# Performance work log

Hardware: AMD Instinct MI355X
Metric: run time of the kernel (lower is better)

## Reference

```python
import jax, jax.numpy as jnp
import numpy as np

B, T, D, H = 8, 1024, 512, 8
HD = D // H
EPS = 1e-5


def setup_inputs() -> dict:
    key = jax.random.key(0)
    ks = jax.random.split(key, 16)
    s = 0.02
    return {
        "query": jax.random.normal(ks[0], (B, T, D), jnp.float32),
        "key": jax.random.normal(ks[1], (B, T, D), jnp.float32),
        "value": jax.random.normal(ks[2], (B, T, D), jnp.float32),
        "frac": jax.random.uniform(ks[3], (B, T), jnp.float32),
        "Wq": jax.random.normal(ks[4], (D, D), jnp.float32) * s,
        "bq": jnp.zeros((D,), jnp.float32),
        "Wk": jax.random.normal(ks[5], (D, D), jnp.float32) * s,
        "bk": jnp.zeros((D,), jnp.float32),
        "Wv": jax.random.normal(ks[6], (D, D), jnp.float32) * s,
        "bv": jnp.zeros((D,), jnp.float32),
        "Wo": jax.random.normal(ks[7], (D, D), jnp.float32) * s,
        "bo": jnp.zeros((D,), jnp.float32),
        # alpha params are zeros in torch init; use small randn so the bias path is non-degenerate
        "alpha_pos": jax.random.normal(ks[8], (H,), jnp.float32) * 0.1,
        "alpha_neg": jax.random.normal(ks[9], (H,), jnp.float32) * 0.1,
        "gamma": jnp.asarray(1.0, jnp.float32),
        "delta": jnp.asarray(0.2, jnp.float32),
        "add_frac_bias": 1,
    }


def _zscore_last(t):
    # torch.std uses unbiased estimator (ddof=1)
    m = t.mean(axis=-1, keepdims=True)
    s = jnp.std(t, axis=-1, keepdims=True, ddof=1)
    return (t - m) / (s + EPS)


def reference(query, key, value, frac, Wq, bq, Wk, bk, Wv, bv, Wo, bo,
              alpha_pos, alpha_neg, gamma, delta, add_frac_bias):
    b, t, d = query.shape
    h = alpha_pos.shape[0]
    hd = d // h
    scale = hd ** -0.5

    def proj(x, W, bias):
        return (x @ W + bias).reshape(b, t, h, hd).transpose(0, 2, 1, 3)  # [B,H,T,hd]

    Q = proj(query, Wq, bq)
    K = proj(key, Wk, bk)
    V = proj(value, Wv, bv)

    logits = jnp.einsum('bhqd,bhkd->bhqk', Q, K) * scale  # [B,H,T,T]

    fi = frac[:, :, None]          # [B,T,1]
    fj = frac[:, None, :]          # [B,1,T]
    Dm = (fj - fi) * (fi * fj)     # [B,T,T]
    D_pos = jax.nn.relu(Dm)
    D_neg = -jax.nn.relu(-Dm)
    stoich = (alpha_pos[None, :, None, None] * D_pos[:, None]
              + alpha_neg[None, :, None, None] * D_neg[:, None])  # [B,H,T,T]

    logits_z = _zscore_last(logits)
    if add_frac_bias:
        attn = gamma * logits_z + delta * _zscore_last(stoich)
    else:
        attn = gamma * logits_z

    probs = jax.nn.softmax(attn, axis=-1)
    out = jnp.einsum('bhqk,bhkd->bhqd', probs, V)  # [B,H,T,hd]
    out = out.transpose(0, 2, 1, 3).reshape(b, t, d)
    return out @ Wo + bo
```

## Files before the change

kernel.cpp:

```cpp
#include <hip/hip_runtime.h>
#include <hip/hip_bf16.h>

#define EPS 1e-5f
#define FLASH_SMEM 72704

typedef short bf16x8 __attribute__((ext_vector_type(8)));
typedef float f32x4 __attribute__((ext_vector_type(4)));

#define GL16(gp, lp) __builtin_amdgcn_global_load_lds( \
    (const __attribute__((address_space(1))) void*)(gp), \
    (__attribute__((address_space(3))) void*)(lp), 16, 0, 0)

__device__ __forceinline__ unsigned short f2bf(float f) {
  union { float f; unsigned u; } v; v.f = f;
  return (unsigned short)((v.u + 0x7FFFu + ((v.u >> 16) & 1u)) >> 16);
}
__device__ __forceinline__ float bf2f(unsigned short u) {
  return __uint_as_float(((unsigned)u) << 16);
}

__global__ void wtrans4_kernel(const float* __restrict__ W0, const float* __restrict__ W1,
                               const float* __restrict__ W2, const float* __restrict__ W3,
                               unsigned short* __restrict__ T0, unsigned short* __restrict__ T1,
                               unsigned short* __restrict__ T2, unsigned short* __restrict__ T3) {
  __shared__ float tile[32][33];
  int z = blockIdx.z;
  const float* W = z == 0 ? W0 : z == 1 ? W1 : z == 2 ? W2 : W3;
  unsigned short* Wt = z == 0 ? T0 : z == 1 ? T1 : z == 2 ? T2 : T3;
  float scale = (z == 0) ? 0.125f : 1.0f;
  int n0 = blockIdx.x * 32, k0 = blockIdx.y * 32;
  int c = threadIdx.x & 31, r0 = threadIdx.x >> 5;
  #pragma unroll
  for (int rr = 0; rr < 32; rr += 8)
    tile[r0 + rr][c] = W[(k0 + r0 + rr) * 512 + n0 + c];
  __syncthreads();
  #pragma unroll
  for (int rr = 0; rr < 32; rr += 8)
    Wt[(n0 + r0 + rr) * 512 + k0 + c] = f2bf(tile[c][r0 + rr] * scale);
}

__global__ void frac_stats_kernel(const float* __restrict__ frac,
                                  float* __restrict__ fstats) {
  int wid = (int)((blockIdx.x * blockDim.x + threadIdx.x) >> 6);
  int ln = threadIdx.x & 63;
  if (wid >= 8192) return;
  int b = wid >> 10, q = wid & 1023;
  const float* fr = frac + b * 1024;
  float fq = fr[q];
  float sp = 0.f, sn = 0.f, sp2 = 0.f, sn2 = 0.f;
  for (int i = ln; i < 1024; i += 64) {
    float f = fr[i];
    float dm = (f - fq) * (fq * f);
    float p = fmaxf(dm, 0.f), nn = fminf(dm, 0.f);
    sp += p; sn += nn; sp2 += p * p; sn2 += nn * nn;
  }
  #pragma unroll
  for (int m = 32; m; m >>= 1) {
    sp += __shfl_xor(sp, m); sn += __shfl_xor(sn, m);
    sp2 += __shfl_xor(sp2, m); sn2 += __shfl_xor(sn2, m);
  }
  if (ln == 0) {
    float4 o; o.x = sp; o.y = sn; o.z = sp2; o.w = sn2;
    *(float4*)(fstats + (size_t)wid * 4) = o;
  }
}

__global__ __launch_bounds__(256) void qkv_gemm_kernel(
    const float* __restrict__ Aq, const float* __restrict__ Ak, const float* __restrict__ Av,
    const unsigned short* __restrict__ WqT, const unsigned short* __restrict__ WkT,
    const unsigned short* __restrict__ WvT,
    const float* __restrict__ bq, const float* __restrict__ bk, const float* __restrict__ bv,
    unsigned short* __restrict__ Qh, unsigned short* __restrict__ Kh,
    unsigned short* __restrict__ Ktr, unsigned short* __restrict__ Vt) {
  __shared__ unsigned short Al[2][128 * 32];
  __shared__ unsigned short Bl[2][128 * 32];
  const int L = blockIdx.x;
  const int xcd = L & 7, sl = L >> 3;
  const int xb = sl & 3;
  const int P = (sl >> 2) * 8 + xcd;
  const int yb = P & 63, z = P >> 6;

  const float* A = z == 0 ? Aq : z == 1 ? Ak : Av;
  const unsigned short* Bt = z == 0 ? WqT : z == 1 ? WkT : WvT;
  const float* bias = z == 0 ? bq : z == 1 ? bk : bv;
  const float bscale = (z == 0) ? 0.125f : 1.0f;

  const int tid = threadIdx.x, ln = tid & 63, wv = tid >> 6;
  const int m0 = yb * 128, n0 = xb * 128;
  const int wr = wv >> 1, wc = wv & 1;
  const int arow = tid >> 1;
  const int agh = (tid & 1) * 2;

  auto stageB = [&](int kt, int buf) {
    int kb = kt * 32;
    #pragma unroll
    for (int u = 0; u < 2; ++u) {
      int n = tid + u * 256;
      int Lrow = n >> 2, kcs = n & 3;
      int kc = kcs ^ (Lrow & 3);
      GL16(Bt + (size_t)(n0 + Lrow) * 512 + kb + kc * 8, &Bl[buf][n * 8]);
    }
  };
  auto loadA = [&](int kt, float4* la) {
    const float* src = A + (size_t)(m0 + arow) * 512 + kt * 32 + agh * 8;
    la[0] = *(const float4*)(src);
    la[1] = *(const float4*)(src + 4);
    la[2] = *(const float4*)(src + 8);
    la[3] = *(const float4*)(src + 12);
  };
  auto writeA = [&](int buf, const float4* la) {
    #pragma unroll
    for (int G = 0; G < 2; ++G) {
      union { bf16x8 v; unsigned short u[8]; } pk;
      float4 a = la[2 * G], b2 = la[2 * G + 1];
      pk.u[0] = f2bf(a.x); pk.u[1] = f2bf(a.y); pk.u[2] = f2bf(a.z); pk.u[3] = f2bf(a.w);
      pk.u[4] = f2bf(b2.x); pk.u[5] = f2bf(b2.y); pk.u[6] = f2bf(b2.z); pk.u[7] = f2bf(b2.w);
      int dg = (agh + G) ^ (arow & 3);
      *(bf16x8*)(&Al[buf][arow * 32 + dg * 8]) = pk.v;
    }
  };

  f32x4 acc[4][4] = {};
  float4 la[4];
  loadA(0, la); writeA(0, la);
  stageB(0, 0);
  for (int kt = 0; kt < 16; ++kt) {
    __syncthreads();
    if (kt < 15) { loadA(kt + 1, la); stageB(kt + 1, (kt + 1) & 1); }
    const unsigned short* a_ = Al[kt & 1];
    const unsigned short* b_ = Bl[kt & 1];
    const int kc = ln >> 4;
    bf16x8 afr[4], bfr[4];
    #pragma unroll
    for (int m = 0; m < 4; ++m) {
      int r = wr * 64 + m * 16 + (ln & 15);
      afr[m] = *(const bf16x8*)(a_ + r * 32 + ((kc ^ (r & 3)) * 8));
    }
    #pragma unroll
    for (int n = 0; n < 4; ++n) {
      int r = wc * 64 + n * 16 + (ln & 15);
      bfr[n] = *(const bf16x8*)(b_ + r * 32 + ((kc ^ (r & 3)) * 8));
    }
    #pragma unroll
    for (int m = 0; m < 4; ++m)
      #pragma unroll
      for (int n = 0; n < 4; ++n)
        acc[m][n] = __builtin_amdgcn_mfma_f32_16x16x32_bf16(afr[m], bfr[n], acc[m][n], 0, 0, 0);
    if (kt < 15) writeA((kt + 1) & 1, la);
  }

  #pragma unroll
  for (int m = 0; m < 4; ++m) {
    #pragma unroll
    for (int n = 0; n < 4; ++n) {
      int gm0 = m0 + wr * 64 + m * 16 + (ln >> 4) * 4;
      int gn = n0 + wc * 64 + n * 16 + (ln & 15);
      float bvv = bias[gn] * bscale;
      int hh = gn >> 6, d = gn & 63;
      if (z < 2) {
        unsigned short* o = z == 0 ? Qh : Kh;
        #pragma unroll
        for (int i = 0; i < 4; ++i) {
          int gm = gm0 + i;
          int bb = gm >> 10, t = gm & 1023;
          o[(size_t)((bb * 8 + hh) * 1024 + t) * 64 + d] = f2bf(acc[m][n][i] + bvv);
        }
        if (z == 1) {
          int bb = gm0 >> 10, t = gm0 & 1023;
          ushort4 pk;
          pk.x = f2bf(acc[m][n][0] + bvv);
          pk.y = f2bf(acc[m][n][1] + bvv);
          pk.z = f2bf(acc[m][n][2] + bvv);
          pk.w = f2bf(acc[m][n][3] + bvv);
          *(ushort4*)(Ktr + (size_t)((bb * 8 + hh) * 64 + d) * 1024 + t) = pk;
        }
      } else {
        int bb = gm0 >> 10, t = gm0 & 1023;
        int k5 = t & 31;
        int pos = (t & ~31) + ((k5 >> 2) & 3) * 8 + ((k5 >> 4) & 1) * 4;
        ushort4 pk;
        pk.x = f2bf(acc[m][n][0] + bvv);
        pk.y = f2bf(acc[m][n][1] + bvv);
        pk.z = f2bf(acc[m][n][2] + bvv);
        pk.w = f2bf(acc[m][n][3] + bvv);
        *(ushort4*)(Vt + (size_t)((bb * 8 + hh) * 64 + d) * 1024 + pos) = pk;
      }
    }
  }
}

__global__ __launch_bounds__(256) void gemm_out_kernel(
    const unsigned short* __restrict__ A,
    const unsigned short* __restrict__ Bt,
    const float* __restrict__ bias,
    float* __restrict__ out) {
  __shared__ unsigned short Al[2][128 * 32];
  __shared__ unsigned short Bl[2][128 * 32];
  const int L = blockIdx.x;
  const int xcd = L & 7, sl = L >> 3;
  const int xb = sl & 3, yb = (sl >> 2) * 8 + xcd;
  const int tid = threadIdx.x, ln = tid & 63, wv = tid >> 6;
  const int m0 = yb * 128, n0 = xb * 128;
  const int wr = wv >> 1, wc = wv & 1;

  auto stage = [&](int kt, int buf) {
    int kb = kt * 32;
    #pragma unroll
    for (int u = 0; u < 2; ++u) {
      int n = tid + u * 256;
      int Lrow = n >> 2, kcs = n & 3;
      int kc = kcs ^ (Lrow & 3);
      GL16(A + (size_t)(m0 + Lrow) * 512 + kb + kc * 8, &Al[buf][n * 8]);
      GL16(Bt + (size_t)(n0 + Lrow) * 512 + kb + kc * 8, &Bl[buf][n * 8]);
    }
  };

  f32x4 acc[4][4] = {};
  stage(0, 0);
  for (int kt = 0; kt < 16; ++kt) {
    __syncthreads();
    if (kt < 15) stage(kt + 1, (kt + 1) & 1);
    const unsigned short* a_ = Al[kt & 1];
    const unsigned short* b_ = Bl[kt & 1];
    const int kc = ln >> 4;
    bf16x8 afr[4], bfr[4];
    #pragma unroll
    for (int m = 0; m < 4; ++m) {
      int r = wr * 64 + m * 16 + (ln & 15);
      afr[m] = *(const bf16x8*)(a_ + r * 32 + ((kc ^ (r & 3)) * 8));
    }
    #pragma unroll
    for (int n = 0; n < 4; ++n) {
      int r = wc * 64 + n * 16 + (ln & 15);
      bfr[n] = *(const bf16x8*)(b_ + r * 32 + ((kc ^ (r & 3)) * 8));
    }
    #pragma unroll
    for (int m = 0; m < 4; ++m)
      #pragma unroll
      for (int n = 0; n < 4; ++n)
        acc[m][n] = __builtin_amdgcn_mfma_f32_16x16x32_bf16(afr[m], bfr[n], acc[m][n], 0, 0, 0);
  }
  #pragma unroll
  for (int m = 0; m < 4; ++m)
    #pragma unroll
    for (int n = 0; n < 4; ++n) {
      int gm0 = m0 + wr * 64 + m * 16 + (ln >> 4) * 4;
      int gn = n0 + wc * 64 + n * 16 + (ln & 15);
      float bvv = bias[gn];
      #pragma unroll
      for (int i = 0; i < 4; ++i)
        out[(size_t)(gm0 + i) * 512 + gn] = acc[m][n][i] + bvv;
    }
}

__global__ __launch_bounds__(256, 1) void gram_kernel(
    const unsigned short* __restrict__ Ktr,
    unsigned short* __restrict__ Mhi, unsigned short* __restrict__ Mlo,
    float* __restrict__ KsumG) {
  __shared__ float KsR[4][64];
  const int bh = blockIdx.x;
  const unsigned short* Kb = Ktr + (size_t)bh * 65536;
  const int tid = threadIdx.x, ln = tid & 63, w = tid >> 6;
  const int c = ln & 15, g = ln >> 4;

  f32x4 acc[4] = {};
  #pragma unroll 2
  for (int kk = 0; kk < 32; ++kk) {
    bf16x8 af = *(const bf16x8*)(Kb + (size_t)(w * 16 + c) * 1024 + kk * 32 + g * 8);
    #pragma unroll
    for (int jt = 0; jt < 4; ++jt) {
      bf16x8 bf = *(const bf16x8*)(Kb + (size_t)(jt * 16 + c) * 1024 + kk * 32 + g * 8);
      acc[jt] = __builtin_amdgcn_mfma_f32_16x16x32_bf16(af, bf, acc[jt], 0, 0, 0);
    }
  }
  #pragma unroll
  for (int jt = 0; jt < 4; ++jt)
    #pragma unroll
    for (int r = 0; r < 4; ++r) {
      float v = acc[jt][r];
      unsigned short hi = f2bf(v);
      unsigned short lo = f2bf(v - bf2f(hi));
      size_t idx = (size_t)bh * 4096 + (w * 16 + g * 4 + r) * 64 + jt * 16 + c;
      Mhi[idx] = hi;
      Mlo[idx] = lo;
    }

  int d = tid & 63, seg = tid >> 6;
  float s = 0.f;
  for (int u = 0; u < 32; ++u) {
    bf16x8 v8 = *(const bf16x8*)(Kb + (size_t)d * 1024 + seg * 256 + u * 8);
    #pragma unroll
    for (int e = 0; e < 8; ++e) s += bf2f((unsigned short)v8[e]);
  }
  KsR[seg][d] = s;
  __syncthreads();
  if (tid < 64)
    KsumG[bh * 64 + tid] = KsR[0][tid] + KsR[1][tid] + KsR[2][tid] + KsR[3][tid];
}

__global__ __launch_bounds__(256) void coef_kernel(
    const unsigned short* __restrict__ Qh,
    const unsigned short* __restrict__ Mhi, const unsigned short* __restrict__ Mlo,
    const float* __restrict__ KsumG,
    const float* __restrict__ frac, const float* __restrict__ fstats,
    const float* __restrict__ alpha_pos, const float* __restrict__ alpha_neg,
    const float* __restrict__ gamma_p, const float* __restrict__ delta_p,
    const int* __restrict__ afb_p,
    float4* __restrict__ rowcG, float* __restrict__ rowShG) {
  const int bh = blockIdx.y;
  const int b = bh >> 3, h = bh & 7;
  const int tid = threadIdx.x, ln = tid & 63, w = tid >> 6;
  const int c = ln & 15, g = ln >> 4;
  const int qrow0 = blockIdx.x * 64 + w * 16;

  const unsigned short* qa = Qh + (size_t)(bh * 1024 + qrow0 + c) * 64 + g * 8;
  bf16x8 aQ0 = *(const bf16x8*)(qa);
  bf16x8 aQ1 = *(const bf16x8*)(qa + 32);

  const unsigned short* Mh = Mhi + (size_t)bh * 4096;
  const unsigned short* Ml = Mlo + (size_t)bh * 4096;
  f32x4 acc[4] = {};
  #pragma unroll
  for (int jt = 0; jt < 4; ++jt) {
    const unsigned short* mrow = Mh + (jt * 16 + c) * 64 + g * 8;
    const unsigned short* lrow = Ml + (jt * 16 + c) * 64 + g * 8;
    bf16x8 bh0 = *(const bf16x8*)(mrow);
    bf16x8 bh1 = *(const bf16x8*)(mrow + 32);
    bf16x8 bl0 = *(const bf16x8*)(lrow);
    bf16x8 bl1 = *(const bf16x8*)(lrow + 32);
    acc[jt] = __builtin_amdgcn_mfma_f32_16x16x32_bf16(aQ0, bh0, acc[jt], 0, 0, 0);
    acc[jt] = __builtin_amdgcn_mfma_f32_16x16x32_bf16(aQ1, bh1, acc[jt], 0, 0, 0);
    acc[jt] = __builtin_amdgcn_mfma_f32_16x16x32_bf16(aQ0, bl0, acc[jt], 0, 0, 0);
    acc[jt] = __builtin_amdgcn_mfma_f32_16x16x32_bf16(aQ1, bl1, acc[jt], 0, 0, 0);
  }

  float ks[4];
  #pragma unroll
  for (int jt = 0; jt < 4; ++jt) ks[jt] = KsumG[bh * 64 + jt * 16 + c];
  float pl[4], p2[4];
  #pragma unroll
  for (int r = 0; r < 4; ++r) {
    const unsigned short* qd = Qh + (size_t)(bh * 1024 + qrow0 + g * 4 + r) * 64 + c;
    float l = 0.f, s2 = 0.f;
    #pragma unroll
    for (int jt = 0; jt < 4; ++jt) {
      float qv = bf2f(qd[jt * 16]);
      s2 += qv * acc[jt][r];
      l += qv * ks[jt];
    }
    pl[r] = l; p2[r] = s2;
  }
  #pragma unroll
  for (int m = 1; m < 16; m <<= 1)
    #pragma unroll
    for (int r = 0; r < 4; ++r) {
      pl[r] += __shfl_xor(pl[r], m);
      p2[r] += __shfl_xor(p2[r], m);
    }

  if (c == 0) {
    const float gmv = *gamma_p, dlv = *delta_p;
    const float ap = alpha_pos[h], an = alpha_neg[h];
    const int afb = *afb_p;
    const float L2E = 1.4426950408889634f;
    #pragma unroll
    for (int r = 0; r < 4; ++r) {
      int q = qrow0 + g * 4 + r;
      float sl = pl[r], sl2 = p2[r];
      float mul_ = sl * (1.f / 1024.f);
      float varl = fmaxf((sl2 - 1024.f * mul_ * mul_) * (1.f / 1023.f), 0.f);
      float cA = gmv / (sqrtf(varl) + EPS);
      float4 st = *(const float4*)(fstats + (size_t)(b * 1024 + q) * 4);
      float msum = ap * st.x + an * st.y;
      float msq = ap * ap * st.z + an * an * st.w;
      float mus = msum * (1.f / 1024.f);
      float vars = fmaxf((msq - 1024.f * mus * mus) * (1.f / 1023.f), 0.f);
      float cB = afb ? (dlv / (sqrtf(vars) + EPS)) : 0.f;
      float4 rc;
      rc.x = frac[b * 1024 + q];
      rc.y = cA * L2E;
      rc.z = cB * ap * L2E;
      rc.w = cB * an * L2E;
      rowcG[(size_t)bh * 1024 + q] = rc;
      rowShG[(size_t)bh * 1024 + q] = (cA * mul_ + cB * mus) * L2E;
    }
  }
}

__global__ __launch_bounds__(256, 2) void flash_kernel(
    const unsigned short* __restrict__ Qh,
    const unsigned short* __restrict__ Kh,
    const unsigned short* __restrict__ Vt,
    unsigned short* __restrict__ attnO,
    const float* __restrict__ frac,
    const float4* __restrict__ rowcG, const float* __restrict__ rowShG) {
  extern __shared__ char smem[];
  unsigned short* Kl = (unsigned short*)smem;
  unsigned short* Vl = (unsigned short*)(smem + 32768);
  float* fk = (float*)(smem + 65536);
  float4* rowcS = (float4*)(smem + 69632);
  float* rowShS = (float*)(smem + 71680);
  float* psumW = (float*)(smem + 72192);

  const int L = blockIdx.x;
  const int xcd = L & 7, s = L >> 3;
  const int bh = xcd + 8 * (s >> 3);
  const int t0 = (s & 7) * 128;
  const int b = bh >> 3, h = bh & 7;
  const int tid = threadIdx.x, ln = tid & 63, w = tid >> 6;
  const int c = ln & 15, g = ln >> 4;

  auto stageK = [&](int t, int buf) {
    #pragma unroll
    for (int u = 0; u < 4; ++u) {
      int n = tid + u * 256;
      int row = n >> 3, kc = (n & 7) ^ (row & 7);
      GL16(Kh + (size_t)(bh * 1024 + t * 128 + row) * 64 + kc * 8,
           Kl + buf * 8192 + n * 8);
    }
  };
  auto stageV = [&](int t, int buf) {
    #pragma unroll
    for (int u = 0; u < 4; ++u) {
      int n = tid + u * 256;
      int d = n >> 4, ch = n & 15;
      GL16(Vt + (size_t)(bh * 64 + d) * 1024 + t * 128 + (ch ^ (d & 15)) * 8,
           Vl + buf * 8192 + n * 8);
    }
  };

  stageK(0, 0);
  stageV(0, 0);
  GL16(frac + b * 1024 + tid * 4, fk + tid * 4);
  if (tid < 128) GL16(rowcG + (size_t)bh * 1024 + t0 + tid, rowcS + tid);
  if (tid < 32) GL16(rowShG + (size_t)bh * 1024 + t0 + tid * 4, rowShS + tid * 4);

  bf16x8 qf[2][2];
  #pragma unroll
  for (int qh = 0; qh < 2; ++qh) {
    const unsigned short* qrow =
        Qh + (size_t)(bh * 1024 + t0 + w * 32 + qh * 16 + c) * 64 + g * 8;
    qf[qh][0] = *(const bf16x8*)(qrow);
    qf[qh][1] = *(const bf16x8*)(qrow + 32);
  }
  __syncthreads();

  const float4 rc0 = rowcS[w * 32 + c], rc1 = rowcS[w * 32 + 16 + c];
  const float sh0 = rowShS[w * 32 + c], sh1 = rowShS[w * 32 + 16 + c];

  f32x4 acc[2][4] = {};
  float ps0a = 0.f, ps0b = 0.f, ps1a = 0.f, ps1b = 0.f;

  for (int t = 0; t < 8; ++t) {
    if (t) __syncthreads();
    if (t < 7) { stageK(t + 1, (t + 1) & 1); stageV(t + 1, (t + 1) & 1); }
    const unsigned short* kb_ = Kl + (t & 1) * 8192;
    const unsigned short* vb_ = Vl + (t & 1) * 8192;

    f32x4 S[8][2];
    #pragma unroll
    for (int kg = 0; kg < 8; ++kg) {
      int krow = kg * 16 + c;
      bf16x8 kf0 = *(const bf16x8*)(kb_ + krow * 64 + ((g ^ (krow & 7)) * 8));
      bf16x8 kf1 = *(const bf16x8*)(kb_ + krow * 64 + (((g + 4) ^ (krow & 7)) * 8));
      #pragma unroll
      for (int qh = 0; qh < 2; ++qh) {
        f32x4 a = {0.f, 0.f, 0.f, 0.f};
        a = __builtin_amdgcn_mfma_f32_16x16x32_bf16(kf0, qf[qh][0], a, 0, 0, 0);
        a = __builtin_amdgcn_mfma_f32_16x16x32_bf16(kf1, qf[qh][1], a, 0, 0, 0);
        S[kg][qh] = a;
      }
    }

    #pragma unroll
    for (int kg = 0; kg < 8; ++kg) {
      float4 f4 = *(const float4*)(&fk[t * 128 + kg * 16 + g * 4]);
      #pragma unroll
      for (int r = 0; r < 4; ++r) {
        float f = (r == 0) ? f4.x : (r == 1) ? f4.y : (r == 2) ? f4.z : f4.w;
        {
          float dd = f - rc0.x, x = f * rc0.x * dd;
          float sel = (dd >= 0.f) ? rc0.z : rc0.w;
          float e = __builtin_amdgcn_exp2f(fmaf(rc0.y, S[kg][0][r], fmaf(x, sel, -sh0)));
          if (kg & 1) ps0a += e; else ps0b += e;
          S[kg][0][r] = e;
        }
        {
          float dd = f - rc1.x, x = f * rc1.x * dd;
          float sel = (dd >= 0.f) ? rc1.z : rc1.w;
          float e = __builtin_amdgcn_exp2f(fmaf(rc1.y, S[kg][1][r], fmaf(x, sel, -sh1)));
          if (kg & 1) ps1a += e; else ps1b += e;
          S[kg][1][r] = e;
        }
      }
    }

    __builtin_amdgcn_s_setprio(1);
    #pragma unroll
    for (int ks = 0; ks < 4; ++ks) {
      union AW { unsigned u[4]; bf16x8 v; } aw0, aw1;
      #pragma unroll
      for (int m = 0; m < 4; ++m) {
        int kg2 = 2 * ks + (m >> 1), rr = (m & 1) * 2;
        unsigned a0 = __float_as_uint(S[kg2][0][rr]), a1 = __float_as_uint(S[kg2][0][rr + 1]);
        aw0.u[m] = ((a1 + 0x8000u) & 0xFFFF0000u) | ((a0 + 0x8000u) >> 16);
        unsigned b0 = __float_as_uint(S[kg2][1][rr]), b1 = __float_as_uint(S[kg2][1][rr + 1]);
        aw1.u[m] = ((b1 + 0x8000u) & 0xFFFF0000u) | ((b0 + 0x8000u) >> 16);
      }
      #pragma unroll
      for (int db = 0; db < 4; ++db) {
        int d = db * 16 + c;
        bf16x8 bv = *(const bf16x8*)(vb_ + d * 128 + (((ks * 4 + g) ^ c) * 8));
        acc[0][db] = __builtin_amdgcn_mfma_f32_16x16x32_bf16(aw0.v, bv, acc[0][db], 0, 0, 0);
        acc[1][db] = __builtin_amdgcn_mfma_f32_16x16x32_bf16(aw1.v, bv, acc[1][db], 0, 0, 0);
      }
    }
    __builtin_amdgcn_s_setprio(0);
  }

  float ps0 = ps0a + ps0b, ps1 = ps1a + ps1b;
  ps0 += __shfl_xor(ps0, 16); ps0 += __shfl_xor(ps0, 32);
  ps1 += __shfl_xor(ps1, 16); ps1 += __shfl_xor(ps1, 32);
  if (g == 0) { psumW[w * 32 + c] = ps0; psumW[w * 32 + 16 + c] = ps1; }

  #pragma unroll
  for (int qh = 0; qh < 2; ++qh)
    #pragma unroll
    for (int r = 0; r < 4; ++r) {
      float rcp = 1.f / psumW[w * 32 + qh * 16 + g * 4 + r];
      int qg = t0 + w * 32 + qh * 16 + g * 4 + r;
      unsigned short* orow = attnO + (size_t)(b * 1024 + qg) * 512 + h * 64 + c;
      #pragma unroll
      for (int db = 0; db < 4; ++db)
        orow[db * 16] = f2bf(acc[qh][db][r] * rcp);
    }
}

extern "C" void kernel_launch(void* const* d_in, const int* in_sizes, int n_in,
                              void* d_out, int out_size, void* d_ws, size_t ws_size,
                              hipStream_t stream) {
  const float* q = (const float*)d_in[0];
  const float* k = (const float*)d_in[1];
  const float* v = (const float*)d_in[2];
  const float* frac = (const float*)d_in[3];
  const float* Wq = (const float*)d_in[4];
  const float* bq = (const float*)d_in[5];
  const float* Wk = (const float*)d_in[6];
  const float* bk = (const float*)d_in[7];
  const float* Wv = (const float*)d_in[8];
  const float* bv = (const float*)d_in[9];
  const float* Wo = (const float*)d_in[10];
  const float* bo = (const float*)d_in[11];
  const float* ap = (const float*)d_in[12];
  const float* an = (const float*)d_in[13];
  const float* gm = (const float*)d_in[14];
  const float* dl = (const float*)d_in[15];
  const int* afb = (const int*)d_in[16];

  char* ws = (char*)d_ws;
  unsigned short* wqT = (unsigned short*)(ws + 0);
  unsigned short* wkT = (unsigned short*)(ws + 524288);
  unsigned short* wvT = (unsigned short*)(ws + 1048576);
  unsigned short* woT = (unsigned short*)(ws + 1572864);
  unsigned short* Qh = (unsigned short*)(ws + 2097152);
  unsigned short* Kh = (unsigned short*)(ws + 10485760);
  unsigned short* Ktr = (unsigned short*)(ws + 18874368);
  unsigned short* Vt = (unsigned short*)(ws + 27262976);
  unsigned short* aO = (unsigned short*)(ws + 35651584);
  float* fst = (float*)(ws + 44040192);
  unsigned short* Mhi = (unsigned short*)(ws + 44171264);
  unsigned short* Mlo = (unsigned short*)(ws + 44695552);
  float* KsumG = (float*)(ws + 45219840);
  float4* rowcG = (float4*)(ws + 45236224);
  float* rowShG = (float*)(ws + 46284800);

  hipFuncSetAttribute((const void*)flash_kernel,
                      hipFuncAttributeMaxDynamicSharedMemorySize, FLASH_SMEM);

  wtrans4_kernel<<<dim3(16, 16, 4), 256, 0, stream>>>(Wq, Wk, Wv, Wo, wqT, wkT, wvT, woT);
  frac_stats_kernel<<<2048, 256, 0, stream>>>(frac, fst);
  qkv_gemm_kernel<<<768, 256, 0, stream>>>(q, k, v, wqT, wkT, wvT,
                                           bq, bk, bv, Qh, Kh, Ktr, Vt);
  gram_kernel<<<64, 256, 0, stream>>>(Ktr, Mhi, Mlo, KsumG);
  coef_kernel<<<dim3(16, 64), 256, 0, stream>>>(Qh, Mhi, Mlo, KsumG, frac, fst,
                                                ap, an, gm, dl, afb, rowcG, rowShG);
  flash_kernel<<<512, 256, FLASH_SMEM, stream>>>(Qh, Kh, Vt, aO, frac, rowcG, rowShG);
  gemm_out_kernel<<<256, 256, 0, stream>>>(aO, woT, bo, (float*)d_out);
}
```

Measured before the change: 129.3 us.

## Halve tile sizes in QKV GEMM and flash kernel to double grid size

The QKV projection GEMM now uses 64-row M tiles instead of 128, launching 1536 blocks rather than 768. The flash attention kernel now processes 64 queries per block with 64-key tiles, launching 1024 blocks, and its shared memory per block roughly halves. The aim is better occupancy and CU load balance on the 256-CU GPU, since the old grids gave only about two or three blocks per CU. The cost is less data reuse per block, so K/V and weight tiles are re-read more often, and the flash kernel has twice as many loop iterations and barriers.

```diff
diff --git a/kernel.cpp b/kernel.cpp
--- a/kernel.cpp
+++ b/kernel.cpp
@@ -2,7 +2,7 @@
 #include <hip/hip_bf16.h>
 
 #define EPS 1e-5f
-#define FLASH_SMEM 72704
+#define FLASH_SMEM 38400
 
 typedef short bf16x8 __attribute__((ext_vector_type(8)));
 typedef float f32x4 __attribute__((ext_vector_type(4)));
@@ -72,13 +72,13 @@
     const float* __restrict__ bq, const float* __restrict__ bk, const float* __restrict__ bv,
     unsigned short* __restrict__ Qh, unsigned short* __restrict__ Kh,
     unsigned short* __restrict__ Ktr, unsigned short* __restrict__ Vt) {
-  __shared__ unsigned short Al[2][128 * 32];
+  __shared__ unsigned short Al[2][64 * 32];
   __shared__ unsigned short Bl[2][128 * 32];
   const int L = blockIdx.x;
   const int xcd = L & 7, sl = L >> 3;
   const int xb = sl & 3;
   const int P = (sl >> 2) * 8 + xcd;
-  const int yb = P & 63, z = P >> 6;
+  const int yb = P & 127, z = P >> 7;
 
   const float* A = z == 0 ? Aq : z == 1 ? Ak : Av;
   const unsigned short* Bt = z == 0 ? WqT : z == 1 ? WkT : WvT;
@@ -86,10 +86,10 @@
   const float bscale = (z == 0) ? 0.125f : 1.0f;
 
   const int tid = threadIdx.x, ln = tid & 63, wv = tid >> 6;
-  const int m0 = yb * 128, n0 = xb * 128;
+  const int m0 = yb * 64, n0 = xb * 128;
   const int wr = wv >> 1, wc = wv & 1;
-  const int arow = tid >> 1;
-  const int agh = (tid & 1) * 2;
+  const int arow = tid >> 2;
+  const int agh = tid & 3;
 
   auto stageB = [&](int kt, int buf) {
     int kb = kt * 32;
@@ -105,23 +105,18 @@
     const float* src = A + (size_t)(m0 + arow) * 512 + kt * 32 + agh * 8;
     la[0] = *(const float4*)(src);
     la[1] = *(const float4*)(src + 4);
-    la[2] = *(const float4*)(src + 8);
-    la[3] = *(const float4*)(src + 12);
   };
   auto writeA = [&](int buf, const float4* la) {
-    #pragma unroll
-    for (int G = 0; G < 2; ++G) {
-      union { bf16x8 v; unsigned short u[8]; } pk;
-      float4 a = la[2 * G], b2 = la[2 * G + 1];
-      pk.u[0] = f2bf(a.x); pk.u[1] = f2bf(a.y); pk.u[2] = f2bf(a.z); pk.u[3] = f2bf(a.w);
-      pk.u[4] = f2bf(b2.x); pk.u[5] = f2bf(b2.y); pk.u[6] = f2bf(b2.z); pk.u[7] = f2bf(b2.w);
-      int dg = (agh + G) ^ (arow & 3);
-      *(bf16x8*)(&Al[buf][arow * 32 + dg * 8]) = pk.v;
-    }
+    union { bf16x8 v; unsigned short u[8]; } pk;
+    float4 a = la[0], b2 = la[1];
+    pk.u[0] = f2bf(a.x); pk.u[1] = f2bf(a.y); pk.u[2] = f2bf(a.z); pk.u[3] = f2bf(a.w);
+    pk.u[4] = f2bf(b2.x); pk.u[5] = f2bf(b2.y); pk.u[6] = f2bf(b2.z); pk.u[7] = f2bf(b2.w);
+    int dg = agh ^ (arow & 3);
+    *(bf16x8*)(&Al[buf][arow * 32 + dg * 8]) = pk.v;
   };
 
-  f32x4 acc[4][4] = {};
-  float4 la[4];
+  f32x4 acc[2][4] = {};
+  float4 la[2];
   loadA(0, la); writeA(0, la);
   stageB(0, 0);
   for (int kt = 0; kt < 16; ++kt) {
@@ -130,10 +125,10 @@
     const unsigned short* a_ = Al[kt & 1];
     const unsigned short* b_ = Bl[kt & 1];
     const int kc = ln >> 4;
-    bf16x8 afr[4], bfr[4];
-    #pragma unroll
-    for (int m = 0; m < 4; ++m) {
-      int r = wr * 64 + m * 16 + (ln & 15);
+    bf16x8 afr[2], bfr[4];
+    #pragma unroll
+    for (int m = 0; m < 2; ++m) {
+      int r = wr * 32 + m * 16 + (ln & 15);
       afr[m] = *(const bf16x8*)(a_ + r * 32 + ((kc ^ (r & 3)) * 8));
     }
     #pragma unroll
@@ -142,7 +137,7 @@
       bfr[n] = *(const bf16x8*)(b_ + r * 32 + ((kc ^ (r & 3)) * 8));
     }
     #pragma unroll
-    for (int m = 0; m < 4; ++m)
+    for (int m = 0; m < 2; ++m)
       #pragma unroll
       for (int n = 0; n < 4; ++n)
         acc[m][n] = __builtin_amdgcn_mfma_f32_16x16x32_bf16(afr[m], bfr[n], acc[m][n], 0, 0, 0);
@@ -150,10 +145,10 @@
   }
 
   #pragma unroll
-  for (int m = 0; m < 4; ++m) {
+  for (int m = 0; m < 2; ++m) {
     #pragma unroll
     for (int n = 0; n < 4; ++n) {
-      int gm0 = m0 + wr * 64 + m * 16 + (ln >> 4) * 4;
+      int gm0 = m0 + wr * 32 + m * 16 + (ln >> 4) * 4;
       int gn = n0 + wc * 64 + n * 16 + (ln & 15);
       float bvv = bias[gn] * bscale;
       int hh = gn >> 6, d = gn & 63;
@@ -396,144 +391,125 @@
     const float4* __restrict__ rowcG, const float* __restrict__ rowShG) {
   extern __shared__ char smem[];
   unsigned short* Kl = (unsigned short*)smem;
-  unsigned short* Vl = (unsigned short*)(smem + 32768);
-  float* fk = (float*)(smem + 65536);
-  float4* rowcS = (float4*)(smem + 69632);
-  float* rowShS = (float*)(smem + 71680);
-  float* psumW = (float*)(smem + 72192);
+  unsigned short* Vl = (unsigned short*)(smem + 16384);
+  float* fk = (float*)(smem + 32768);
+  float4* rowcS = (float4*)(smem + 36864);
+  float* rowShS = (float*)(smem + 37888);
+  float* psumW = (float*)(smem + 38144);
 
   const int L = blockIdx.x;
   const int xcd = L & 7, s = L >> 3;
-  const int bh = xcd + 8 * (s >> 3);
-  const int t0 = (s & 7) * 128;
+  const int bh = xcd + 8 * (s >> 4);
+  const int t0 = (s & 15) * 64;
   const int b = bh >> 3, h = bh & 7;
   const int tid = threadIdx.x, ln = tid & 63, w = tid >> 6;
   const int c = ln & 15, g = ln >> 4;
 
   auto stageK = [&](int t, int buf) {
     #pragma unroll
-    for (int u = 0; u < 4; ++u) {
+    for (int u = 0; u < 2; ++u) {
       int n = tid + u * 256;
       int row = n >> 3, kc = (n & 7) ^ (row & 7);
-      GL16(Kh + (size_t)(bh * 1024 + t * 128 + row) * 64 + kc * 8,
-           Kl + buf * 8192 + n * 8);
+      GL16(Kh + (size_t)(bh * 1024 + t * 64 + row) * 64 + kc * 8,
+           Kl + buf * 4096 + n * 8);
     }
   };
   auto stageV = [&](int t, int buf) {
     #pragma unroll
-    for (int u = 0; u < 4; ++u) {
+    for (int u = 0; u < 2; ++u) {
       int n = tid + u * 256;
-      int d = n >> 4, ch = n & 15;
-      GL16(Vt + (size_t)(bh * 64 + d) * 1024 + t * 128 + (ch ^ (d & 15)) * 8,
-           Vl + buf * 8192 + n * 8);
+      int d = n >> 3, ch = n & 7;
+      GL16(Vt + (size_t)(bh * 64 + d) * 1024 + t * 64 + (ch ^ (d & 7)) * 8,
+           Vl + buf * 4096 + n * 8);
     }
   };
 
   stageK(0, 0);
   stageV(0, 0);
   GL16(frac + b * 1024 + tid * 4, fk + tid * 4);
-  if (tid < 128) GL16(rowcG + (size_t)bh * 1024 + t0 + tid, rowcS + tid);
-  if (tid < 32) GL16(rowShG + (size_t)bh * 1024 + t0 + tid * 4, rowShS + tid * 4);
-
-  bf16x8 qf[2][2];
-  #pragma unroll
-  for (int qh = 0; qh < 2; ++qh) {
+  if (tid < 64) GL16(rowcG + (size_t)bh * 1024 + t0 + tid, rowcS + tid);
+  if (tid < 16) GL16(rowShG + (size_t)bh * 1024 + t0 + tid * 4, rowShS + tid * 4);
+
+  bf16x8 qf0, qf1;
+  {
     const unsigned short* qrow =
-        Qh + (size_t)(bh * 1024 + t0 + w * 32 + qh * 16 + c) * 64 + g * 8;
-    qf[qh][0] = *(const bf16x8*)(qrow);
-    qf[qh][1] = *(const bf16x8*)(qrow + 32);
+        Qh + (size_t)(bh * 1024 + t0 + w * 16 + c) * 64 + g * 8;
+    qf0 = *(const bf16x8*)(qrow);
+    qf1 = *(const bf16x8*)(qrow + 32);
   }
   __syncthreads();
 
-  const float4 rc0 = rowcS[w * 32 + c], rc1 = rowcS[w * 32 + 16 + c];
-  const float sh0 = rowShS[w * 32 + c], sh1 = rowShS[w * 32 + 16 + c];
-
-  f32x4 acc[2][4] = {};
-  float ps0a = 0.f, ps0b = 0.f, ps1a = 0.f, ps1b = 0.f;
-
-  for (int t = 0; t < 8; ++t) {
+  const float4 rc = rowcS[w * 16 + c];
+  const float sh = rowShS[w * 16 + c];
+
+  f32x4 acc[4] = {};
+  float psa = 0.f, psb = 0.f;
+
+  for (int t = 0; t < 16; ++t) {
     if (t) __syncthreads();
-    if (t < 7) { stageK(t + 1, (t + 1) & 1); stageV(t + 1, (t + 1) & 1); }
-    const unsigned short* kb_ = Kl + (t & 1) * 8192;
-    const unsigned short* vb_ = Vl + (t & 1) * 8192;
-
-    f32x4 S[8][2];
-    #pragma unroll
-    for (int kg = 0; kg < 8; ++kg) {
+    if (t < 15) { stageK(t + 1, (t + 1) & 1); stageV(t + 1, (t + 1) & 1); }
+    const unsigned short* kb_ = Kl + (t & 1) * 4096;
+    const unsigned short* vb_ = Vl + (t & 1) * 4096;
+
+    f32x4 S[4];
+    #pragma unroll
+    for (int kg = 0; kg < 4; ++kg) {
       int krow = kg * 16 + c;
       bf16x8 kf0 = *(const bf16x8*)(kb_ + krow * 64 + ((g ^ (krow & 7)) * 8));
       bf16x8 kf1 = *(const bf16x8*)(kb_ + krow * 64 + (((g + 4) ^ (krow & 7)) * 8));
-      #pragma unroll
-      for (int qh = 0; qh < 2; ++qh) {
-        f32x4 a = {0.f, 0.f, 0.f, 0.f};
-        a = __builtin_amdgcn_mfma_f32_16x16x32_bf16(kf0, qf[qh][0], a, 0, 0, 0);
-        a = __builtin_amdgcn_mfma_f32_16x16x32_bf16(kf1, qf[qh][1], a, 0, 0, 0);
-        S[kg][qh] = a;
-      }
-    }
-
-    #pragma unroll
-    for (int kg = 0; kg < 8; ++kg) {
-      float4 f4 = *(const float4*)(&fk[t * 128 + kg * 16 + g * 4]);
+      f32x4 a = {0.f, 0.f, 0.f, 0.f};
+      a = __builtin_amdgcn_mfma_f32_16x16x32_bf16(kf0, qf0, a, 0, 0, 0);
+      a = __builtin_amdgcn_mfma_f32_16x16x32_bf16(kf1, qf1, a, 0, 0, 0);
+      S[kg] = a;
+    }
+
+    #pragma unroll
+    for (int kg = 0; kg < 4; ++kg) {
+      float4 f4 = *(const float4*)(&fk[t * 64 + kg * 16 + g * 4]);
       #pragma unroll
       for (int r = 0; r < 4; ++r) {
         float f = (r == 0) ? f4.x : (r == 1) ? f4.y : (r == 2) ? f4.z : f4.w;
-        {
-          float dd = f - rc0.x, x = f * rc0.x * dd;
-          float sel = (dd >= 0.f) ? rc0.z : rc0.w;
-          float e = __builtin_amdgcn_exp2f(fmaf(rc0.y, S[kg][0][r], fmaf(x, sel, -sh0)));
-          if (kg & 1) ps0a += e; else ps0b += e;
-          S[kg][0][r] = e;
-        }
-        {
-          float dd = f - rc1.x, x = f * rc1.x * dd;
-          float sel = (dd >= 0.f) ? rc1.z : rc1.w;
-          float e = __builtin_amdgcn_exp2f(fmaf(rc1.y, S[kg][1][r], fmaf(x, sel, -sh1)));
-          if (kg & 1) ps1a += e; else ps1b += e;
-          S[kg][1][r] = e;
-        }
+        float dd = f - rc.x, x = f * rc.x * dd;
+        float sel = (dd >= 0.f) ? rc.z : rc.w;
+        float e = __builtin_amdgcn_exp2f(fmaf(rc.y, S[kg][r], fmaf(x, sel, -sh)));
+        if (kg & 1) psa += e; else psb += e;
+        S[kg][r] = e;
       }
     }
 
     __builtin_amdgcn_s_setprio(1);
     #pragma unroll
-    for (int ks = 0; ks < 4; ++ks) {
-      union AW { unsigned u[4]; bf16x8 v; } aw0, aw1;
+    for (int ks = 0; ks < 2; ++ks) {
+      union AW { unsigned u[4]; bf16x8 v; } aw;
       #pragma unroll
       for (int m = 0; m < 4; ++m) {
         int kg2 = 2 * ks + (m >> 1), rr = (m & 1) * 2;
-        unsigned a0 = __float_as_uint(S[kg2][0][rr]), a1 = __float_as_uint(S[kg2][0][rr + 1]);
-        aw0.u[m] = ((a1 + 0x8000u) & 0xFFFF0000u) | ((a0 + 0x8000u) >> 16);
-        unsigned b0 = __float_as_uint(S[kg2][1][rr]), b1 = __float_as_uint(S[kg2][1][rr + 1]);
-        aw1.u[m] = ((b1 + 0x8000u) & 0xFFFF0000u) | ((b0 + 0x8000u) >> 16);
+        unsigned a0 = __float_as_uint(S[kg2][rr]), a1 = __float_as_uint(S[kg2][rr + 1]);
+        aw.u[m] = ((a1 + 0x8000u) & 0xFFFF0000u) | ((a0 + 0x8000u) >> 16);
       }
       #pragma unroll
       for (int db = 0; db < 4; ++db) {
         int d = db * 16 + c;
-        bf16x8 bv = *(const bf16x8*)(vb_ + d * 128 + (((ks * 4 + g) ^ c) * 8));
-        acc[0][db] = __builtin_amdgcn_mfma_f32_16x16x32_bf16(aw0.v, bv, acc[0][db], 0, 0, 0);
-        acc[1][db] = __builtin_amdgcn_mfma_f32_16x16x32_bf16(aw1.v, bv, acc[1][db], 0, 0, 0);
+        bf16x8 bv = *(const bf16x8*)(vb_ + d * 64 + (((ks * 4 + g) ^ (d & 7)) * 8));
+        acc[db] = __builtin_amdgcn_mfma_f32_16x16x32_bf16(aw.v, bv, acc[db], 0, 0, 0);
       }
     }
     __builtin_amdgcn_s_setprio(0);
   }
 
-  float ps0 = ps0a + ps0b, ps1 = ps1a + ps1b;
-  ps0 += __shfl_xor(ps0, 16); ps0 += __shfl_xor(ps0, 32);
-  ps1 += __shfl_xor(ps1, 16); ps1 += __shfl_xor(ps1, 32);
-  if (g == 0) { psumW[w * 32 + c] = ps0; psumW[w * 32 + 16 + c] = ps1; }
-
-  #pragma unroll
-  for (int qh = 0; qh < 2; ++qh)
-    #pragma unroll
-    for (int r = 0; r < 4; ++r) {
-      float rcp = 1.f / psumW[w * 32 + qh * 16 + g * 4 + r];
-      int qg = t0 + w * 32 + qh * 16 + g * 4 + r;
-      unsigned short* orow = attnO + (size_t)(b * 1024 + qg) * 512 + h * 64 + c;
-      #pragma unroll
-      for (int db = 0; db < 4; ++db)
-        orow[db * 16] = f2bf(acc[qh][db][r] * rcp);
-    }
+  float ps = psa + psb;
+  ps += __shfl_xor(ps, 16); ps += __shfl_xor(ps, 32);
+  if (g == 0) psumW[w * 16 + c] = ps;
+
+  #pragma unroll
+  for (int r = 0; r < 4; ++r) {
+    float rcp = 1.f / psumW[w * 16 + g * 4 + r];
+    int qg = t0 + w * 16 + g * 4 + r;
+    unsigned short* orow = attnO + (size_t)(b * 1024 + qg) * 512 + h * 64 + c;
+    #pragma unroll
+    for (int db = 0; db < 4; ++db)
+      orow[db * 16] = f2bf(acc[db][r] * rcp);
+  }
 }
 
 extern "C" void kernel_launch(void* const* d_in, const int* in_sizes, int n_in,
@@ -579,11 +555,11 @@
 
   wtrans4_kernel<<<dim3(16, 16, 4), 256, 0, stream>>>(Wq, Wk, Wv, Wo, wqT, wkT, wvT, woT);
   frac_stats_kernel<<<2048, 256, 0, stream>>>(frac, fst);
-  qkv_gemm_kernel<<<768, 256, 0, stream>>>(q, k, v, wqT, wkT, wvT,
-                                           bq, bk, bv, Qh, Kh, Ktr, Vt);
+  qkv_gemm_kernel<<<1536, 256, 0, stream>>>(q, k, v, wqT, wkT, wvT,
+                                            bq, bk, bv, Qh, Kh, Ktr, Vt);
   gram_kernel<<<64, 256, 0, stream>>>(Ktr, Mhi, Mlo, KsumG);
   coef_kernel<<<dim3(16, 64), 256, 0, stream>>>(Qh, Mhi, Mlo, KsumG, frac, fst,
                                                 ap, an, gm, dl, afb, rowcG, rowShG);
-  flash_kernel<<<512, 256, FLASH_SMEM, stream>>>(Qh, Kh, Vt, aO, frac, rowcG, rowShG);
+  flash_kernel<<<1024, 256, FLASH_SMEM, stream>>>(Qh, Kh, Vt, aO, frac, rowcG, rowShG);
   gemm_out_kernel<<<256, 256, 0, stream>>>(aO, woT, bo, (float*)d_out);
 }
```

New measurement: 134.1 us. +3.7%, slower.
